# Optimization experiments

Measured on AMD Instinct MI355X. Metric: run time of the kernel, lower is better.

The kernel has to match this reference:

```python
import jax, jax.numpy as jnp
import numpy as np


def setup_inputs() -> dict:
    key = jax.random.key(0)
    z = jax.random.normal(key, (8, 4096, 1024), dtype=jnp.float32)
    return {"z": z}


def reference(z):
    d = z.shape[-1]
    # sort descending along last dim
    z_sorted = -jnp.sort(-z, axis=-1)
    z_cumsum = jnp.cumsum(z_sorted, axis=-1)
    k = jnp.arange(1, d + 1, dtype=z.dtype)  # [d]
    rhs = 1 + k * z_sorted
    is_gt = (rhs > z_cumsum).astype(z.dtype)
    # largest k satisfying the support condition
    k_z = jnp.max(is_gt * k, axis=-1, keepdims=True)  # [..., 1]
    idx = k_z.astype(jnp.int32) - 1
    z_cumsum_k = jnp.take_along_axis(z_cumsum, idx, axis=-1)
    tau = (z_cumsum_k - 1) / k_z
    p = jnp.clip(z - tau, 0.0, None)
    return p
```

## Files before the change

### kernel.cpp

```cpp
#include <hip/hip_runtime.h>


#define ROW_D 1024

__device__ __forceinline__ float wave_allreduce_sum(float v) {
#pragma unroll
    for (int off = 1; off < 64; off <<= 1)
        v += __shfl_xor(v, off, 64);
    return v;
}

__device__ __forceinline__ float wave_allreduce_max(float v) {
#pragma unroll
    for (int off = 1; off < 64; off <<= 1)
        v = fmaxf(v, __shfl_xor(v, off, 64));
    return v;
}

__global__ __launch_bounds__(256) void sparsemax_kernel(
    const float* __restrict__ z, float* __restrict__ out, int nrows) {
    const int gwave = (int)((blockIdx.x * 256u + threadIdx.x) >> 6);
    const int lane  = (int)(threadIdx.x & 63u);
    if (gwave >= nrows) return;

    const float4* __restrict__ zin  =
        reinterpret_cast<const float4*>(z + (size_t)gwave * ROW_D);
    float4* __restrict__ pout =
        reinterpret_cast<float4*>(out + (size_t)gwave * ROW_D);

    float4 v[4];
#pragma unroll
    for (int j = 0; j < 4; ++j) v[j] = zin[lane + 64 * j];

    float m = fmaxf(fmaxf(v[0].x, v[0].y), fmaxf(v[0].z, v[0].w));
#pragma unroll
    for (int j = 1; j < 4; ++j)
        m = fmaxf(m, fmaxf(fmaxf(v[j].x, v[j].y), fmaxf(v[j].z, v[j].w)));
    m = wave_allreduce_max(m);

    float lo = m - 1.0f, hi = m;
#pragma unroll
    for (int it = 0; it < 20; ++it) {
        const float tau = 0.5f * (lo + hi);
        float s = 0.0f;
#pragma unroll
        for (int j = 0; j < 4; ++j) {
            s += fmaxf(v[j].x - tau, 0.0f);
            s += fmaxf(v[j].y - tau, 0.0f);
            s += fmaxf(v[j].z - tau, 0.0f);
            s += fmaxf(v[j].w - tau, 0.0f);
        }
        s = wave_allreduce_sum(s);
        if (s >= 1.0f) lo = tau; else hi = tau;
    }

    float s = 0.0f, k = 0.0f;
#pragma unroll
    for (int j = 0; j < 4; ++j) {
        float e;
        e = v[j].x; if (e > lo) { s += e; k += 1.0f; }
        e = v[j].y; if (e > lo) { s += e; k += 1.0f; }
        e = v[j].z; if (e > lo) { s += e; k += 1.0f; }
        e = v[j].w; if (e > lo) { s += e; k += 1.0f; }
    }
    s = wave_allreduce_sum(s);
    k = wave_allreduce_sum(k);
    float tau = (s - 1.0f) / k;
    tau = fminf(fmaxf(tau, lo), hi);

#pragma unroll
    for (int j = 0; j < 4; ++j) {
        float4 o;
        o.x = fmaxf(v[j].x - tau, 0.0f);
        o.y = fmaxf(v[j].y - tau, 0.0f);
        o.z = fmaxf(v[j].z - tau, 0.0f);
        o.w = fmaxf(v[j].w - tau, 0.0f);
        pout[lane + 64 * j] = o;
    }
}

extern "C" void kernel_launch(void* const* d_in, const int* in_sizes, int n_in,
                              void* d_out, int out_size, void* d_ws, size_t ws_size,
                              hipStream_t stream) {
    const float* z = (const float*)d_in[0];
    float* out = (float*)d_out;
    const int n = in_sizes[0];
    const int nrows = n / ROW_D;
    const int blocks = (nrows + 3) / 4;
    sparsemax_kernel<<<blocks, 256, 0, stream>>>(z, out, nrows);
}
```

Before: 230.8 us.

## Compact candidates above max-1 into LDS and bisect on the small set

```diff
diff --git a/kernel.cpp b/kernel.cpp
--- a/kernel.cpp
+++ b/kernel.cpp
@@ -2,31 +2,33 @@
 
 
 #define ROW_D 1024
+#define CAP   128
+#define NEG_PAD -3.0e38f
 
-__device__ __forceinline__ float wave_allreduce_sum(float v) {
+__device__ __forceinline__ float wsum(float v) {
 #pragma unroll
-    for (int off = 1; off < 64; off <<= 1)
-        v += __shfl_xor(v, off, 64);
+    for (int off = 1; off < 64; off <<= 1) v += __shfl_xor(v, off, 64);
     return v;
 }
-
-__device__ __forceinline__ float wave_allreduce_max(float v) {
+__device__ __forceinline__ float wmax(float v) {
 #pragma unroll
-    for (int off = 1; off < 64; off <<= 1)
-        v = fmaxf(v, __shfl_xor(v, off, 64));
+    for (int off = 1; off < 64; off <<= 1) v = fmaxf(v, __shfl_xor(v, off, 64));
     return v;
 }
 
 __global__ __launch_bounds__(256) void sparsemax_kernel(
     const float* __restrict__ z, float* __restrict__ out, int nrows) {
-    const int gwave = (int)((blockIdx.x * 256u + threadIdx.x) >> 6);
+    const int wslot = (int)(threadIdx.x >> 6);
     const int lane  = (int)(threadIdx.x & 63u);
-    if (gwave >= nrows) return;
+    int row = (int)(blockIdx.x << 2) + wslot;
+    if (row >= nrows) row = nrows - 1;
 
-    const float4* __restrict__ zin  =
-        reinterpret_cast<const float4*>(z + (size_t)gwave * ROW_D);
+    __shared__ float cbuf[4][CAP];
+
+    const float4* __restrict__ zin =
+        reinterpret_cast<const float4*>(z + (size_t)row * ROW_D);
     float4* __restrict__ pout =
-        reinterpret_cast<float4*>(out + (size_t)gwave * ROW_D);
+        reinterpret_cast<float4*>(out + (size_t)row * ROW_D);
 
     float4 v[4];
 #pragma unroll
@@ -36,37 +38,72 @@
 #pragma unroll
     for (int j = 1; j < 4; ++j)
         m = fmaxf(m, fmaxf(fmaxf(v[j].x, v[j].y), fmaxf(v[j].z, v[j].w)));
-    m = wave_allreduce_max(m);
+    m = wmax(m);
+    const float lo0 = m - 1.0f;
 
-    float lo = m - 1.0f, hi = m;
+    cbuf[wslot][lane]      = NEG_PAD;
+    cbuf[wslot][lane + 64] = NEG_PAD;
+    const unsigned long long ltmask = (1ULL << lane) - 1ULL;
+    int base = 0;
 #pragma unroll
-    for (int it = 0; it < 20; ++it) {
-        const float tau = 0.5f * (lo + hi);
-        float s = 0.0f;
+    for (int j = 0; j < 4; ++j) {
+        const float e[4] = {v[j].x, v[j].y, v[j].z, v[j].w};
+#pragma unroll
+        for (int c = 0; c < 4; ++c) {
+            const bool cand = e[c] > lo0;
+            const unsigned long long b = __ballot(cand);
+            const int pos = base + __popcll(b & ltmask);
+            if (cand && pos < CAP) cbuf[wslot][pos] = e[c];
+            base += __popcll(b);
+        }
+    }
+    __syncthreads();
+    const int K = base;
+
+    float tau;
+    if (K <= CAP) {
+        const float x0 = cbuf[wslot][lane];
+        const float x1 = cbuf[wslot][lane + 64];
+        float lo = lo0, hi = m;
+#pragma unroll
+        for (int it = 0; it < 12; ++it) {
+            const float t = 0.5f * (lo + hi);
+            float s = fmaxf(x0 - t, 0.0f) + fmaxf(x1 - t, 0.0f);
+            s = wsum(s);
+            if (s >= 1.0f) lo = t; else hi = t;
+        }
+        float s = 0.0f, k = 0.0f;
+        if (x0 > lo) { s += x0; k += 1.0f; }
+        if (x1 > lo) { s += x1; k += 1.0f; }
+        s = wsum(s); k = wsum(k);
+        tau = fminf(fmaxf((s - 1.0f) / k, lo), hi);
+    } else {
+        float lo = lo0, hi = m;
+        for (int it = 0; it < 24; ++it) {
+            const float t = 0.5f * (lo + hi);
+            float s = 0.0f;
+#pragma unroll
+            for (int j = 0; j < 4; ++j) {
+                s += fmaxf(v[j].x - t, 0.0f);
+                s += fmaxf(v[j].y - t, 0.0f);
+                s += fmaxf(v[j].z - t, 0.0f);
+                s += fmaxf(v[j].w - t, 0.0f);
+            }
+            s = wsum(s);
+            if (s >= 1.0f) lo = t; else hi = t;
+        }
+        float s = 0.0f, k = 0.0f;
 #pragma unroll
         for (int j = 0; j < 4; ++j) {
-            s += fmaxf(v[j].x - tau, 0.0f);
-            s += fmaxf(v[j].y - tau, 0.0f);
-            s += fmaxf(v[j].z - tau, 0.0f);
-            s += fmaxf(v[j].w - tau, 0.0f);
+            float e;
+            e = v[j].x; if (e > lo) { s += e; k += 1.0f; }
+            e = v[j].y; if (e > lo) { s += e; k += 1.0f; }
+            e = v[j].z; if (e > lo) { s += e; k += 1.0f; }
+            e = v[j].w; if (e > lo) { s += e; k += 1.0f; }
         }
-        s = wave_allreduce_sum(s);
-        if (s >= 1.0f) lo = tau; else hi = tau;
+        s = wsum(s); k = wsum(k);
+        tau = fminf(fmaxf((s - 1.0f) / k, lo), hi);
     }
-
-    float s = 0.0f, k = 0.0f;
-#pragma unroll
-    for (int j = 0; j < 4; ++j) {
-        float e;
-        e = v[j].x; if (e > lo) { s += e; k += 1.0f; }
-        e = v[j].y; if (e > lo) { s += e; k += 1.0f; }
-        e = v[j].z; if (e > lo) { s += e; k += 1.0f; }
-        e = v[j].w; if (e > lo) { s += e; k += 1.0f; }
-    }
-    s = wave_allreduce_sum(s);
-    k = wave_allreduce_sum(k);
-    float tau = (s - 1.0f) / k;
-    tau = fminf(fmaxf(tau, lo), hi);
 
 #pragma unroll
     for (int j = 0; j < 4; ++j) {
```

New measurement: 230.0 us. Within noise of the previous version (-0.3%).

## Compact sparsemax candidates via ballot and iterate tau on two rows per wave

Applied to the files above, without the earlier changes.

```diff
diff --git a/kernel.cpp b/kernel.cpp
--- a/kernel.cpp
+++ b/kernel.cpp
@@ -2,58 +2,50 @@
 
 
 #define ROW_D 1024
+#define NEG_PAD -3.0e38f
 
-__device__ __forceinline__ float wave_allreduce_sum(float v) {
+__device__ __forceinline__ void wsum4(float& a, float& b, float& c, float& d) {
 #pragma unroll
-    for (int off = 1; off < 64; off <<= 1)
-        v += __shfl_xor(v, off, 64);
+    for (int off = 1; off < 64; off <<= 1) {
+        a += __shfl_xor(a, off, 64);
+        b += __shfl_xor(b, off, 64);
+        c += __shfl_xor(c, off, 64);
+        d += __shfl_xor(d, off, 64);
+    }
+}
+__device__ __forceinline__ void wmax2(float& a, float& b) {
+#pragma unroll
+    for (int off = 1; off < 64; off <<= 1) {
+        a = fmaxf(a, __shfl_xor(a, off, 64));
+        b = fmaxf(b, __shfl_xor(b, off, 64));
+    }
+}
+__device__ __forceinline__ float wsum1(float v) {
+#pragma unroll
+    for (int off = 1; off < 64; off <<= 1) v += __shfl_xor(v, off, 64);
     return v;
 }
 
-__device__ __forceinline__ float wave_allreduce_max(float v) {
-#pragma unroll
-    for (int off = 1; off < 64; off <<= 1)
-        v = fmaxf(v, __shfl_xor(v, off, 64));
-    return v;
-}
-
-__global__ __launch_bounds__(256) void sparsemax_kernel(
-    const float* __restrict__ z, float* __restrict__ out, int nrows) {
-    const int gwave = (int)((blockIdx.x * 256u + threadIdx.x) >> 6);
-    const int lane  = (int)(threadIdx.x & 63u);
-    if (gwave >= nrows) return;
-
-    const float4* __restrict__ zin  =
-        reinterpret_cast<const float4*>(z + (size_t)gwave * ROW_D);
-    float4* __restrict__ pout =
-        reinterpret_cast<float4*>(out + (size_t)gwave * ROW_D);
-
-    float4 v[4];
-#pragma unroll
-    for (int j = 0; j < 4; ++j) v[j] = zin[lane + 64 * j];
-
+__device__ __forceinline__ float row_max16(const float4* v) {
     float m = fmaxf(fmaxf(v[0].x, v[0].y), fmaxf(v[0].z, v[0].w));
 #pragma unroll
     for (int j = 1; j < 4; ++j)
         m = fmaxf(m, fmaxf(fmaxf(v[j].x, v[j].y), fmaxf(v[j].z, v[j].w)));
-    m = wave_allreduce_max(m);
+    return m;
+}
 
-    float lo = m - 1.0f, hi = m;
-#pragma unroll
-    for (int it = 0; it < 20; ++it) {
-        const float tau = 0.5f * (lo + hi);
+__device__ __forceinline__ float full_bisect(const float4* v, float lo, float hi) {
+    for (int it = 0; it < 24; ++it) {
+        const float t = 0.5f * (lo + hi);
         float s = 0.0f;
 #pragma unroll
         for (int j = 0; j < 4; ++j) {
-            s += fmaxf(v[j].x - tau, 0.0f);
-            s += fmaxf(v[j].y - tau, 0.0f);
-            s += fmaxf(v[j].z - tau, 0.0f);
-            s += fmaxf(v[j].w - tau, 0.0f);
+            s += fmaxf(v[j].x - t, 0.0f) + fmaxf(v[j].y - t, 0.0f);
+            s += fmaxf(v[j].z - t, 0.0f) + fmaxf(v[j].w - t, 0.0f);
         }
-        s = wave_allreduce_sum(s);
-        if (s >= 1.0f) lo = tau; else hi = tau;
+        s = wsum1(s);
+        if (s >= 1.0f) lo = t; else hi = t;
     }
-
     float s = 0.0f, k = 0.0f;
 #pragma unroll
     for (int j = 0; j < 4; ++j) {
@@ -63,19 +55,98 @@
         e = v[j].z; if (e > lo) { s += e; k += 1.0f; }
         e = v[j].w; if (e > lo) { s += e; k += 1.0f; }
     }
-    s = wave_allreduce_sum(s);
-    k = wave_allreduce_sum(k);
-    float tau = (s - 1.0f) / k;
-    tau = fminf(fmaxf(tau, lo), hi);
+    s = wsum1(s); k = wsum1(k);
+    return fminf(fmaxf((s - 1.0f) / k, lo), hi);
+}
 
+__global__ __launch_bounds__(256) void sparsemax_kernel(
+    const float* __restrict__ z, float* __restrict__ out, int nrows) {
+    const int wslot = (int)(threadIdx.x >> 6);
+    const int lane  = (int)(threadIdx.x & 63u);
+    const int ra = (int)(blockIdx.x << 3) + (wslot << 1);
+    if (ra >= nrows) return;
+    const int rb = (ra + 1 < nrows) ? ra + 1 : ra;
+
+    __shared__ float cbuf[4][2][64];
+
+    const float4* __restrict__ za =
+        reinterpret_cast<const float4*>(z + (size_t)ra * ROW_D);
+    const float4* __restrict__ zb =
+        reinterpret_cast<const float4*>(z + (size_t)rb * ROW_D);
+
+    float4 va[4], vb[4];
+#pragma unroll
+    for (int j = 0; j < 4; ++j) va[j] = za[lane + 64 * j];
+#pragma unroll
+    for (int j = 0; j < 4; ++j) vb[j] = zb[lane + 64 * j];
+
+    float ma = row_max16(va), mb = row_max16(vb);
+    wmax2(ma, mb);
+    const float loa = ma - 1.0f, lob = mb - 1.0f;
+
+    cbuf[wslot][0][lane] = NEG_PAD;
+    cbuf[wslot][1][lane] = NEG_PAD;
+    int Ka = 0, Kb = 0;
 #pragma unroll
     for (int j = 0; j < 4; ++j) {
-        float4 o;
-        o.x = fmaxf(v[j].x - tau, 0.0f);
-        o.y = fmaxf(v[j].y - tau, 0.0f);
-        o.z = fmaxf(v[j].z - tau, 0.0f);
-        o.w = fmaxf(v[j].w - tau, 0.0f);
-        pout[lane + 64 * j] = o;
+        const float ea[4] = {va[j].x, va[j].y, va[j].z, va[j].w};
+        const float eb[4] = {vb[j].x, vb[j].y, vb[j].z, vb[j].w};
+#pragma unroll
+        for (int c = 0; c < 4; ++c) {
+            {
+                const bool cand = ea[c] > loa;
+                const unsigned long long b = __ballot(cand);
+                const int pre = (int)__builtin_amdgcn_mbcnt_hi(
+                    (unsigned)(b >> 32),
+                    __builtin_amdgcn_mbcnt_lo((unsigned)b, 0u));
+                const int pos = Ka + pre;
+                if (cand && pos < 64) cbuf[wslot][0][pos] = ea[c];
+                Ka += __popcll(b);
+            }
+            {
+                const bool cand = eb[c] > lob;
+                const unsigned long long b = __ballot(cand);
+                const int pre = (int)__builtin_amdgcn_mbcnt_hi(
+                    (unsigned)(b >> 32),
+                    __builtin_amdgcn_mbcnt_lo((unsigned)b, 0u));
+                const int pos = Kb + pre;
+                if (cand && pos < 64) cbuf[wslot][1][pos] = eb[c];
+                Kb += __popcll(b);
+            }
+        }
+    }
+    const float ca = cbuf[wslot][0][lane];
+    const float cb = cbuf[wslot][1][lane];
+
+    float ta, tb;
+    if (Ka <= 64 && Kb <= 64) {
+        ta = loa; tb = lob;
+        for (int it = 0; it < 16; ++it) {
+            float sa = (ca > ta) ? ca : 0.0f, na = (ca > ta) ? 1.0f : 0.0f;
+            float sb = (cb > tb) ? cb : 0.0f, nb = (cb > tb) ? 1.0f : 0.0f;
+            wsum4(sa, na, sb, nb);
+            const float ta2 = (sa - 1.0f) / na;
+            const float tb2 = (sb - 1.0f) / nb;
+            const bool done = (ta2 == ta) && (tb2 == tb);
+            ta = ta2; tb = tb2;
+            if (done) break;
+        }
+    } else {
+        ta = full_bisect(va, loa, ma);
+        tb = full_bisect(vb, lob, mb);
+    }
+
+    float4* __restrict__ pa = reinterpret_cast<float4*>(out + (size_t)ra * ROW_D);
+    float4* __restrict__ pb = reinterpret_cast<float4*>(out + (size_t)rb * ROW_D);
+#pragma unroll
+    for (int j = 0; j < 4; ++j) {
+        float4 oa, ob;
+        oa.x = fmaxf(va[j].x - ta, 0.0f); oa.y = fmaxf(va[j].y - ta, 0.0f);
+        oa.z = fmaxf(va[j].z - ta, 0.0f); oa.w = fmaxf(va[j].w - ta, 0.0f);
+        ob.x = fmaxf(vb[j].x - tb, 0.0f); ob.y = fmaxf(vb[j].y - tb, 0.0f);
+        ob.z = fmaxf(vb[j].z - tb, 0.0f); ob.w = fmaxf(vb[j].w - tb, 0.0f);
+        pa[lane + 64 * j] = oa;
+        pb[lane + 64 * j] = ob;
     }
 }
 
@@ -86,6 +157,6 @@
     float* out = (float*)d_out;
     const int n = in_sizes[0];
     const int nrows = n / ROW_D;
-    const int blocks = (nrows + 3) / 4;
+    const int blocks = (nrows + 7) / 8;
     sparsemax_kernel<<<blocks, 256, 0, stream>>>(z, out, nrows);
 }
```

Measured after the change: 239.2 us. +3.6%, slower.

## Replace bisection with Michelot-style fixed-point iteration and DPP wave reductions

Applied to the files above, without the earlier changes.

```diff
diff --git a/kernel.cpp b/kernel.cpp
--- a/kernel.cpp
+++ b/kernel.cpp
@@ -3,79 +3,88 @@
 
 #define ROW_D 1024
 
-__device__ __forceinline__ float wave_allreduce_sum(float v) {
-#pragma unroll
-    for (int off = 1; off < 64; off <<= 1)
-        v += __shfl_xor(v, off, 64);
-    return v;
+typedef float f4 __attribute__((ext_vector_type(4)));
+
+template <int CTRL, int RMASK>
+__device__ __forceinline__ float dpp_mv(float x) {
+    return __builtin_bit_cast(float, __builtin_amdgcn_update_dpp(
+        __builtin_bit_cast(int, x), __builtin_bit_cast(int, x),
+        CTRL, RMASK, 0xf, false));
 }
 
-__device__ __forceinline__ float wave_allreduce_max(float v) {
-#pragma unroll
-    for (int off = 1; off < 64; off <<= 1)
-        v = fmaxf(v, __shfl_xor(v, off, 64));
-    return v;
+__device__ __forceinline__ float dpp_sum_to63(float x) {
+    x += dpp_mv<0x111, 0xf>(x);
+    x += dpp_mv<0x112, 0xf>(x);
+    x += dpp_mv<0x114, 0xf>(x);
+    x += dpp_mv<0x118, 0xf>(x);
+    x += dpp_mv<0x142, 0xa>(x);
+    x += dpp_mv<0x143, 0xc>(x);
+    return x;
+}
+__device__ __forceinline__ float dpp_max_to63(float x) {
+    x = fmaxf(x, dpp_mv<0x111, 0xf>(x));
+    x = fmaxf(x, dpp_mv<0x112, 0xf>(x));
+    x = fmaxf(x, dpp_mv<0x114, 0xf>(x));
+    x = fmaxf(x, dpp_mv<0x118, 0xf>(x));
+    x = fmaxf(x, dpp_mv<0x142, 0xa>(x));
+    x = fmaxf(x, dpp_mv<0x143, 0xc>(x));
+    return x;
+}
+__device__ __forceinline__ float bcast63(float x) {
+    return __builtin_bit_cast(float,
+        __builtin_amdgcn_readlane(__builtin_bit_cast(int, x), 63));
 }
 
 __global__ __launch_bounds__(256) void sparsemax_kernel(
     const float* __restrict__ z, float* __restrict__ out, int nrows) {
-    const int gwave = (int)((blockIdx.x * 256u + threadIdx.x) >> 6);
-    const int lane  = (int)(threadIdx.x & 63u);
-    if (gwave >= nrows) return;
+    const int lane = (int)(threadIdx.x & 63u);
+    const int row  = (int)(blockIdx.x << 2) + (int)(threadIdx.x >> 6);
+    if (row >= nrows) return;
 
-    const float4* __restrict__ zin  =
-        reinterpret_cast<const float4*>(z + (size_t)gwave * ROW_D);
-    float4* __restrict__ pout =
-        reinterpret_cast<float4*>(out + (size_t)gwave * ROW_D);
+    const f4* __restrict__ zin = reinterpret_cast<const f4*>(z + (size_t)row * ROW_D);
+    f4* __restrict__ pout      = reinterpret_cast<f4*>(out + (size_t)row * ROW_D);
 
-    float4 v[4];
+    f4 v[4];
 #pragma unroll
     for (int j = 0; j < 4; ++j) v[j] = zin[lane + 64 * j];
 
-    float m = fmaxf(fmaxf(v[0].x, v[0].y), fmaxf(v[0].z, v[0].w));
+    float mj[4];
 #pragma unroll
-    for (int j = 1; j < 4; ++j)
-        m = fmaxf(m, fmaxf(fmaxf(v[j].x, v[j].y), fmaxf(v[j].z, v[j].w)));
-    m = wave_allreduce_max(m);
+    for (int j = 0; j < 4; ++j)
+        mj[j] = fmaxf(fmaxf(v[j].x, v[j].y), fmaxf(v[j].z, v[j].w));
+    float m = fmaxf(fmaxf(mj[0], mj[1]), fmaxf(mj[2], mj[3]));
+    m = bcast63(dpp_max_to63(m));
 
-    float lo = m - 1.0f, hi = m;
-#pragma unroll
-    for (int it = 0; it < 20; ++it) {
-        const float tau = 0.5f * (lo + hi);
-        float s = 0.0f;
+    float t = m - 1.0f;
+#pragma unroll 1
+    for (int it = 0; it < 16; ++it) {
+        float sj[4];
+        int n = 0;
 #pragma unroll
         for (int j = 0; j < 4; ++j) {
-            s += fmaxf(v[j].x - tau, 0.0f);
-            s += fmaxf(v[j].y - tau, 0.0f);
-            s += fmaxf(v[j].z - tau, 0.0f);
-            s += fmaxf(v[j].w - tau, 0.0f);
+            const float d0 = v[j].x - t, d1 = v[j].y - t;
+            const float d2 = v[j].z - t, d3 = v[j].w - t;
+            sj[j] = (fmaxf(d0, 0.0f) + fmaxf(d1, 0.0f)) +
+                    (fmaxf(d2, 0.0f) + fmaxf(d3, 0.0f));
+            n += __popcll(__ballot(d0 > 0.0f));
+            n += __popcll(__ballot(d1 > 0.0f));
+            n += __popcll(__ballot(d2 > 0.0f));
+            n += __popcll(__ballot(d3 > 0.0f));
         }
-        s = wave_allreduce_sum(s);
-        if (s >= 1.0f) lo = tau; else hi = tau;
+        float S = bcast63(dpp_sum_to63((sj[0] + sj[1]) + (sj[2] + sj[3])));
+        const float t2 = t + (S - 1.0f) / (float)n;
+        if (t2 - t <= 1e-6f) { t = t2; break; }
+        t = t2;
     }
-
-    float s = 0.0f, k = 0.0f;
-#pragma unroll
-    for (int j = 0; j < 4; ++j) {
-        float e;
-        e = v[j].x; if (e > lo) { s += e; k += 1.0f; }
-        e = v[j].y; if (e > lo) { s += e; k += 1.0f; }
-        e = v[j].z; if (e > lo) { s += e; k += 1.0f; }
-        e = v[j].w; if (e > lo) { s += e; k += 1.0f; }
-    }
-    s = wave_allreduce_sum(s);
-    k = wave_allreduce_sum(k);
-    float tau = (s - 1.0f) / k;
-    tau = fminf(fmaxf(tau, lo), hi);
 
 #pragma unroll
     for (int j = 0; j < 4; ++j) {
-        float4 o;
-        o.x = fmaxf(v[j].x - tau, 0.0f);
-        o.y = fmaxf(v[j].y - tau, 0.0f);
-        o.z = fmaxf(v[j].z - tau, 0.0f);
-        o.w = fmaxf(v[j].w - tau, 0.0f);
-        pout[lane + 64 * j] = o;
+        f4 o;
+        o.x = fmaxf(v[j].x - t, 0.0f);
+        o.y = fmaxf(v[j].y - t, 0.0f);
+        o.z = fmaxf(v[j].z - t, 0.0f);
+        o.w = fmaxf(v[j].w - t, 0.0f);
+        __builtin_nontemporal_store(o, pout + lane + 64 * j);
     }
 }
 
```

Result: no change. 229.1 us (-0.7%).
